# Kernel optimization log

Measured on AMD Instinct MI355X. Metric: run time of the kernel, lower is better.

The kernel has to match this reference:

```python
import jax, jax.numpy as jnp
import numpy as np

NUM_HEADS = 16


def setup_inputs() -> dict:
    key = jax.random.key(0)
    ks = jax.random.split(key, 8)
    B, T, E = 2, 2048, 1024
    hd = E // NUM_HEADS
    return {
        "x": jax.random.normal(ks[0], (B, T, E), jnp.float32),
        "attn_mask_re": jax.random.normal(ks[1], (B, 1, T, hd // 2), jnp.float32),
        "attn_mask_im": jax.random.normal(ks[2], (B, 1, T, hd // 2), jnp.float32),
        "pad_mask": jax.random.normal(ks[3], (B, 1, 1, T), jnp.float32),
        "qkv_w": jax.random.normal(ks[4], (3 * E, E), jnp.float32) * 0.02,
        "qkv_b": jax.random.normal(ks[5], (3 * E,), jnp.float32) * 0.02,
        "o_w": jax.random.normal(ks[6], (E, E), jnp.float32) * 0.02,
        "o_b": jax.random.normal(ks[7], (E,), jnp.float32) * 0.02,
    }


def reference(x, attn_mask_re, attn_mask_im, pad_mask, qkv_w, qkv_b, o_w, o_b):
    B, T, E = x.shape
    H = NUM_HEADS
    hd = E // H
    scale = 1.0 / jnp.sqrt(jnp.asarray(hd, x.dtype))
    # fused QKV projection
    qkv = x @ qkv_w.T + qkv_b            # [B,T,3E]
    q, k, v = jnp.split(qkv, 3, axis=-1)
    q = q.reshape(B, T, H, hd).transpose(0, 2, 1, 3)          # [B,H,T,hd]
    v = v.reshape(B, T, H, hd).transpose(0, 2, 1, 3)          # [B,H,T,hd]
    # rotary on k via complex multiply: k viewed as [B,H,T,hd/2] complex
    kc = k.reshape(B, T, H, hd // 2, 2).transpose(0, 2, 1, 3, 4)  # [B,H,T,hd/2,2]
    kr, ki = kc[..., 0], kc[..., 1]
    mr, mi = attn_mask_re, attn_mask_im   # [B,1,T,hd/2] broadcast over heads
    rr = kr * mr - ki * mi
    ri = kr * mi + ki * mr
    k_rot = jnp.stack([rr, ri], axis=-1).reshape(B, H, T, hd)  # [B,H,T,hd]
    # attention scores [B,H,T,T]
    a = jnp.einsum("bhqd,bhkd->bhqk", q, k_rot) * scale
    a = a + pad_mask
    a = jax.nn.softmax(a, axis=-1)
    # (eval mode: attention dropout is a no-op)
    o = jnp.einsum("bhqk,bhkd->bhqd", a, v)                    # [B,H,T,hd]
    o = o.transpose(0, 2, 1, 3).reshape(B, T, E)
    o = o @ o_w.T + o_b
    a_avg = a.sum(axis=1) / H                                  # [B,T,T]
    return o, a_avg
```

## Files before the change

kernel.cpp:

```cpp
#include <hip/hip_runtime.h>
#include <math.h>

#define TSEQ 2048
#define EMB  1024
#define NH   16
#define HD   64
#define NB   2
#define L2E  1.4426950408889634f

#if defined(__has_builtin)
#if __has_builtin(__builtin_amdgcn_exp2f)
#define EXP2(x) __builtin_amdgcn_exp2f(x)
#else
#define EXP2(x) exp2f(x)
#endif
#else
#define EXP2(x) exp2f(x)
#endif

typedef unsigned short u16;
typedef unsigned int   u32;
typedef __attribute__((ext_vector_type(8))) short short8v;
typedef __attribute__((ext_vector_type(4))) float f32x4;

#define MFMA16(a,b,c) __builtin_amdgcn_mfma_f32_16x16x32_bf16(a,b,c,0,0,0)

__device__ inline u32 f2bf(float x) {
    u32 u = __float_as_uint(x);
    return (u + 0x7fffu + ((u >> 16) & 1u)) >> 16;
}
__device__ inline float bf2f(u32 b) { return __uint_as_float(b << 16); }
__device__ inline void split4(float x0, float x1, float x2, float x3,
                              u32& hw0, u32& hw1, u32& lw0, u32& lw1) {
    u32 h0 = f2bf(x0), h1 = f2bf(x1), h2 = f2bf(x2), h3 = f2bf(x3);
    u32 l0 = f2bf(x0 - bf2f(h0)), l1 = f2bf(x1 - bf2f(h1));
    u32 l2 = f2bf(x2 - bf2f(h2)), l3 = f2bf(x3 - bf2f(h3));
    hw0 = h0 | (h1 << 16); hw1 = h2 | (h3 << 16);
    lw0 = l0 | (l1 << 16); lw1 = l2 | (l3 << 16);
}

__global__ __launch_bounds__(256) void conv_split_kernel(
    const float* __restrict__ in, u16* __restrict__ hi, u16* __restrict__ lo)
{
    const size_t i = (size_t)blockIdx.x * 256 + threadIdx.x;
    float4 v = ((const float4*)in)[i];
    u32 hw0, hw1, lw0, lw1;
    split4(v.x, v.y, v.z, v.w, hw0, hw1, lw0, lw1);
    *(uint2*)(hi + i * 4) = make_uint2(hw0, hw1);
    *(uint2*)(lo + i * 4) = make_uint2(lw0, lw1);
}

#define MM_CORE(Ah_, Al_, Bh_, Bl_, Kdim)                                      \
    __shared__ __align__(16) u16 sAh[128][40], sAl[128][40];                   \
    __shared__ __align__(16) u16 sBh[128][40], sBl[128][40];                   \
    const int tid = threadIdx.x;                                               \
    const int lane = tid & 63, w = tid >> 6;                                   \
    const int lc = lane & 15, lg = lane >> 4;                                  \
    const int wr = w >> 1, wc = w & 1;                                         \
    const int i0 = blockIdx.x * 128, j0 = blockIdx.y * 128;                    \
    const int srow = tid >> 1, shalf = (tid & 1) << 4;                         \
    const u16* pAh = Ah_ + (size_t)(i0 + srow) * Kdim + shalf;                 \
    const u16* pAl = Al_ + (size_t)(i0 + srow) * Kdim + shalf;                 \
    const u16* pBh = Bh_ + (size_t)(j0 + srow) * Kdim + shalf;                 \
    const u16* pBl = Bl_ + (size_t)(j0 + srow) * Kdim + shalf;                 \
    f32x4 acc[4][4];                                                           \
    _Pragma("unroll")                                                          \
    for (int rs = 0; rs < 4; ++rs)                                             \
        _Pragma("unroll")                                                      \
        for (int cs = 0; cs < 4; ++cs) acc[rs][cs] = (f32x4){0.f,0.f,0.f,0.f};\
    for (int k0 = 0; k0 < Kdim; k0 += 32) {                                    \
        short8v va0 = *(const short8v*)(pAh + k0);                             \
        short8v va1 = *(const short8v*)(pAh + k0 + 8);                         \
        short8v vb0 = *(const short8v*)(pAl + k0);                             \
        short8v vb1 = *(const short8v*)(pAl + k0 + 8);                         \
        short8v vc0 = *(const short8v*)(pBh + k0);                             \
        short8v vc1 = *(const short8v*)(pBh + k0 + 8);                         \
        short8v vd0 = *(const short8v*)(pBl + k0);                             \
        short8v vd1 = *(const short8v*)(pBl + k0 + 8);                         \
        *(short8v*)&sAh[srow][shalf]     = va0;                                \
        *(short8v*)&sAh[srow][shalf + 8] = va1;                                \
        *(short8v*)&sAl[srow][shalf]     = vb0;                                \
        *(short8v*)&sAl[srow][shalf + 8] = vb1;                                \
        *(short8v*)&sBh[srow][shalf]     = vc0;                                \
        *(short8v*)&sBh[srow][shalf + 8] = vc1;                                \
        *(short8v*)&sBl[srow][shalf]     = vd0;                                \
        *(short8v*)&sBl[srow][shalf + 8] = vd1;                                \
        __syncthreads();                                                       \
        short8v fah[4], fal[4], fbh[4], fbl[4];                                \
        _Pragma("unroll")                                                      \
        for (int rs = 0; rs < 4; ++rs) {                                       \
            fah[rs] = *(const short8v*)&sAh[wr*64 + rs*16 + lc][lg*8];         \
            fal[rs] = *(const short8v*)&sAl[wr*64 + rs*16 + lc][lg*8];         \
        }                                                                      \
        _Pragma("unroll")                                                      \
        for (int cs = 0; cs < 4; ++cs) {                                       \
            fbh[cs] = *(const short8v*)&sBh[wc*64 + cs*16 + lc][lg*8];         \
            fbl[cs] = *(const short8v*)&sBl[wc*64 + cs*16 + lc][lg*8];         \
        }                                                                      \
        _Pragma("unroll")                                                      \
        for (int rs = 0; rs < 4; ++rs)                                         \
            _Pragma("unroll")                                                  \
            for (int cs = 0; cs < 4; ++cs) {                                   \
                acc[rs][cs] = MFMA16(fah[rs], fbh[cs], acc[rs][cs]);           \
                acc[rs][cs] = MFMA16(fah[rs], fbl[cs], acc[rs][cs]);           \
                acc[rs][cs] = MFMA16(fal[rs], fbh[cs], acc[rs][cs]);           \
            }                                                                  \
        __syncthreads();                                                       \
    }

__global__ __launch_bounds__(256) void mm_qkv_kernel(
    const u16* __restrict__ Ah, const u16* __restrict__ Al,
    const u16* __restrict__ Bh, const u16* __restrict__ Bl,
    const float* __restrict__ bias,
    u16* __restrict__ qhi, u16* __restrict__ qlo,
    u16* __restrict__ khi, u16* __restrict__ klo,
    u16* __restrict__ vthi, u16* __restrict__ vtlo)
{
    MM_CORE(Ah, Al, Bh, Bl, EMB)

    const int which = j0 >> 10;
    #pragma unroll
    for (int cs = 0; cs < 4; ++cs) {
        const int j = j0 + wc*64 + cs*16 + lc;
        const float bj = bias[j];
        const int e = j & (EMB - 1);
        const int hh = e >> 6, d = e & (HD - 1);
        #pragma unroll
        for (int rs = 0; rs < 4; ++rs) {
            #pragma unroll
            for (int r = 0; r < 4; ++r) {
                const int i = i0 + wr*64 + rs*16 + lg*4 + r;
                const int b = i >> 11, t = i & (TSEQ - 1);
                float val = acc[rs][cs][r] + bj;
                if (which == 0) val *= 0.125f;
                const u32 vh = f2bf(val);
                const u32 vl = f2bf(val - bf2f(vh));
                if (which == 2) {
                    const size_t ix = ((size_t)(b * NH + hh) * HD + d) * TSEQ + t;
                    vthi[ix] = (u16)vh; vtlo[ix] = (u16)vl;
                } else {
                    const size_t ix = ((size_t)(b * NH + hh) * TSEQ + t) * HD + d;
                    if (which == 0) { qhi[ix] = (u16)vh; qlo[ix] = (u16)vl; }
                    else            { khi[ix] = (u16)vh; klo[ix] = (u16)vl; }
                }
            }
        }
    }
}

__global__ __launch_bounds__(256) void mm_out_kernel(
    const u16* __restrict__ Ah, const u16* __restrict__ Al,
    const u16* __restrict__ Bh, const u16* __restrict__ Bl,
    const float* __restrict__ bias, float* __restrict__ C)
{
    MM_CORE(Ah, Al, Bh, Bl, EMB)

    #pragma unroll
    for (int cs = 0; cs < 4; ++cs) {
        const int j = j0 + wc*64 + cs*16 + lc;
        const float bj = bias[j];
        #pragma unroll
        for (int rs = 0; rs < 4; ++rs) {
            #pragma unroll
            for (int r = 0; r < 4; ++r) {
                const int i = i0 + wr*64 + rs*16 + lg*4 + r;
                C[(size_t)i * EMB + j] = acc[rs][cs][r] + bj;
            }
        }
    }
}

__global__ __launch_bounds__(256) void rotary_k_kernel(
    u16* __restrict__ khi, u16* __restrict__ klo,
    const float* __restrict__ mre, const float* __restrict__ mim)
{
    const int idx = blockIdx.x * 256 + threadIdx.x;
    const int d2 = idx & 31;
    const int t  = (idx >> 5) & (TSEQ - 1);
    const int b  = idx >> 20;
    u32 h2 = *(u32*)(khi + ((size_t)idx << 1));
    u32 l2 = *(u32*)(klo + ((size_t)idx << 1));
    float kr = bf2f(h2 & 0xffff) + bf2f(l2 & 0xffff);
    float ki = bf2f(h2 >> 16) + bf2f(l2 >> 16);
    const int mix = (b * TSEQ + t) * 32 + d2;
    const float mr = mre[mix], mi = mim[mix];
    float rr = kr * mr - ki * mi;
    float ri = kr * mi + ki * mr;
    u32 hr = f2bf(rr), hx = f2bf(ri);
    u32 lr = f2bf(rr - bf2f(hr)), lx = f2bf(ri - bf2f(hx));
    *(u32*)(khi + ((size_t)idx << 1)) = hr | (hx << 16);
    *(u32*)(klo + ((size_t)idx << 1)) = lr | (lx << 16);
}

__global__ __launch_bounds__(128) void flash_attn_kernel(
    const u16* __restrict__ qhi_, const u16* __restrict__ qlo_,
    const u16* __restrict__ khi_, const u16* __restrict__ klo_,
    const u16* __restrict__ vthi_, const u16* __restrict__ vtlo_,
    const float* __restrict__ pad,
    u16* __restrict__ ohi, u16* __restrict__ olo,
    float* __restrict__ m_out, float* __restrict__ linv_out)
{
    __shared__ __align__(16) u16 Phi[2][32*40];
    __shared__ __align__(16) u16 Plo[2][32*40];

    const int tid  = threadIdx.x;
    const int lane = tid & 63;
    const int w    = tid >> 6;
    const int bid  = blockIdx.x;
    const int xcd  = bid & 7;
    const int local= bid >> 3;
    const int bh   = xcd * 4 + (local >> 5);
    const int sub  = local & 31;
    const int b    = bh >> 4, h = bh & (NH - 1);
    const int qbase = sub * 64 + w * 32;
    const int lg = lane >> 4, lc = lane & 15;

    short8v qh[2][2], ql[2][2];
    #pragma unroll
    for (int qs = 0; qs < 2; ++qs) {
        const size_t qoff = ((size_t)bh * TSEQ + qbase + qs*16 + lc) * HD + lg*8;
        #pragma unroll
        for (int s = 0; s < 2; ++s) {
            qh[qs][s] = *(const short8v*)(qhi_ + qoff + s*32);
            ql[qs][s] = *(const short8v*)(qlo_ + qoff + s*32);
        }
    }

    f32x4 O[2][4];
    float mst[2][4], lst[2][4];
    #pragma unroll
    for (int qs = 0; qs < 2; ++qs) {
        #pragma unroll
        for (int db = 0; db < 4; ++db) O[qs][db] = (f32x4){0.f,0.f,0.f,0.f};
        #pragma unroll
        for (int r = 0; r < 4; ++r) { mst[qs][r] = -1e30f; lst[qs][r] = 0.f; }
    }

    const short oneb = (short)0x3F80;
    const short8v ones = {oneb,oneb,oneb,oneb,oneb,oneb,oneb,oneb};

    u16* PHw = &Phi[w][0];
    u16* PLw = &Plo[w][0];
    const size_t kbase  = (size_t)bh * TSEQ * HD;
    const size_t vtbase = (size_t)bh * HD * TSEQ;

    for (int k0 = 0; k0 < TSEQ; k0 += 32) {
        f32x4 S[2][2];
        #pragma unroll
        for (int qs = 0; qs < 2; ++qs)
            #pragma unroll
            for (int kb2 = 0; kb2 < 2; ++kb2) S[qs][kb2] = (f32x4){0.f,0.f,0.f,0.f};
        #pragma unroll
        for (int kb2 = 0; kb2 < 2; ++kb2) {
            #pragma unroll
            for (int s = 0; s < 2; ++s) {
                const size_t ko = kbase + (size_t)(k0 + kb2*16 + lc) * HD + s*32 + lg*8;
                short8v kh = *(const short8v*)(khi_ + ko);
                short8v kl = *(const short8v*)(klo_ + ko);
                #pragma unroll
                for (int qs = 0; qs < 2; ++qs) {
                    S[qs][kb2] = MFMA16(qh[qs][s], kh, S[qs][kb2]);
                    S[qs][kb2] = MFMA16(qh[qs][s], kl, S[qs][kb2]);
                    S[qs][kb2] = MFMA16(ql[qs][s], kh, S[qs][kb2]);
                }
            }
        }

        short8v vh[4], vl[4];
        #pragma unroll
        for (int db = 0; db < 4; ++db) {
            const size_t vo = vtbase + (size_t)(db*16 + lc) * TSEQ + k0 + lg*8;
            vh[db] = *(const short8v*)(vthi_ + vo);
            vl[db] = *(const short8v*)(vtlo_ + vo);
        }

        const float pv0 = pad[b * TSEQ + k0 + lc];
        const float pv1 = pad[b * TSEQ + k0 + 16 + lc];

        float cc_[2][4];
        #pragma unroll
        for (int qs = 0; qs < 2; ++qs) {
            #pragma unroll
            for (int r = 0; r < 4; ++r) {
                float s0 = S[qs][0][r] + pv0;
                float s1 = S[qs][1][r] + pv1;
                float t = fmaxf(s0, s1);
                t = fmaxf(t, __shfl_xor(t, 1));
                t = fmaxf(t, __shfl_xor(t, 2));
                t = fmaxf(t, __shfl_xor(t, 4));
                t = fmaxf(t, __shfl_xor(t, 8));
                const float mn = fmaxf(mst[qs][r], t);
                cc_[qs][r] = EXP2((mst[qs][r] - mn) * L2E);
                mst[qs][r] = mn;
                const float p0 = EXP2((s0 - mn) * L2E);
                const float p1 = EXP2((s1 - mn) * L2E);
                const int row = qs*16 + lg*4 + r;
                const u32 h0 = f2bf(p0), h1 = f2bf(p1);
                PHw[row*40 + lc]      = (u16)h0;
                PHw[row*40 + 16 + lc] = (u16)h1;
                PLw[row*40 + lc]      = (u16)f2bf(p0 - bf2f(h0));
                PLw[row*40 + 16 + lc] = (u16)f2bf(p1 - bf2f(h1));
                #pragma unroll
                for (int db = 0; db < 4; ++db) O[qs][db][r] *= cc_[qs][r];
            }
        }

        short8v pfh[2], pfl[2];
        #pragma unroll
        for (int qs = 0; qs < 2; ++qs) {
            pfh[qs] = *(const short8v*)(PHw + (qs*16 + lc)*40 + lg*8);
            pfl[qs] = *(const short8v*)(PLw + (qs*16 + lc)*40 + lg*8);
        }

        #pragma unroll
        for (int qs = 0; qs < 2; ++qs) {
            f32x4 Ss = (f32x4){0.f,0.f,0.f,0.f};
            Ss = MFMA16(pfh[qs], ones, Ss);
            Ss = MFMA16(pfl[qs], ones, Ss);
            #pragma unroll
            for (int r = 0; r < 4; ++r) lst[qs][r] = lst[qs][r] * cc_[qs][r] + Ss[r];
        }

        #pragma unroll
        for (int db = 0; db < 4; ++db) {
            #pragma unroll
            for (int qs = 0; qs < 2; ++qs) {
                O[qs][db] = MFMA16(pfh[qs], vh[db], O[qs][db]);
                O[qs][db] = MFMA16(pfh[qs], vl[db], O[qs][db]);
                O[qs][db] = MFMA16(pfl[qs], vh[db], O[qs][db]);
            }
        }
    }

    #pragma unroll
    for (int qs = 0; qs < 2; ++qs) {
        #pragma unroll
        for (int r = 0; r < 4; ++r) {
            const float inv = 1.f / lst[qs][r];
            const int trow = qbase + qs*16 + lg*4 + r;
            const size_t obase = ((size_t)(b * TSEQ + trow)) * EMB + h * HD;
            #pragma unroll
            for (int db = 0; db < 4; ++db) {
                const float val = O[qs][db][r] * inv;
                const u32 vhp = f2bf(val);
                ohi[obase + db*16 + lc] = (u16)vhp;
                olo[obase + db*16 + lc] = (u16)f2bf(val - bf2f(vhp));
            }
            if (lc == 0) {
                m_out[bh * TSEQ + trow] = mst[qs][r];
                linv_out[bh * TSEQ + trow] = inv;
            }
        }
    }
}

__global__ __launch_bounds__(256) void attn_avg_kernel(
    const u16* __restrict__ qhi_, const u16* __restrict__ qlo_,
    const u16* __restrict__ khi_, const u16* __restrict__ klo_,
    const float* __restrict__ pad, const float* __restrict__ m_arr,
    const float* __restrict__ linv_arr, float* __restrict__ a_avg)
{
    const int tid  = threadIdx.x;
    const int lane = tid & 63;
    const int w    = tid >> 6;
    const int bid  = blockIdx.x;
    const int xcd  = bid & 7;
    const int local= bid >> 3;
    const int pair = xcd * 4 + (local >> 6);
    const int b  = pair >> 4;
    const int k0 = (pair & 15) << 7;
    const int q0 = (local & 63) << 5;
    const int lg = lane >> 4, lc = lane & 15;
    const int kw = k0 + w * 32;

    const float pv0 = pad[b * TSEQ + kw + lc];
    const float pv1 = pad[b * TSEQ + kw + 16 + lc];

    f32x4 acc[2][2];
    #pragma unroll
    for (int qs = 0; qs < 2; ++qs)
        #pragma unroll
        for (int kb2 = 0; kb2 < 2; ++kb2) acc[qs][kb2] = (f32x4){0.f,0.f,0.f,0.f};

    for (int h = 0; h < NH; ++h) {
        const size_t hb = (size_t)(b * NH + h) * TSEQ;
        short8v qh[2][2], ql[2][2];
        #pragma unroll
        for (int qs = 0; qs < 2; ++qs) {
            const size_t qoff = (hb + q0 + qs*16 + lc) * HD + lg*8;
            #pragma unroll
            for (int s = 0; s < 2; ++s) {
                qh[qs][s] = *(const short8v*)(qhi_ + qoff + s*32);
                ql[qs][s] = *(const short8v*)(qlo_ + qoff + s*32);
            }
        }
        f32x4 S[2][2];
        #pragma unroll
        for (int qs = 0; qs < 2; ++qs)
            #pragma unroll
            for (int kb2 = 0; kb2 < 2; ++kb2) S[qs][kb2] = (f32x4){0.f,0.f,0.f,0.f};
        #pragma unroll
        for (int kb2 = 0; kb2 < 2; ++kb2) {
            #pragma unroll
            for (int s = 0; s < 2; ++s) {
                const size_t ko = (hb + kw + kb2*16 + lc) * HD + s*32 + lg*8;
                short8v kh = *(const short8v*)(khi_ + ko);
                short8v kl = *(const short8v*)(klo_ + ko);
                #pragma unroll
                for (int qs = 0; qs < 2; ++qs) {
                    S[qs][kb2] = MFMA16(qh[qs][s], kh, S[qs][kb2]);
                    S[qs][kb2] = MFMA16(qh[qs][s], kl, S[qs][kb2]);
                    S[qs][kb2] = MFMA16(ql[qs][s], kh, S[qs][kb2]);
                }
            }
        }
        #pragma unroll
        for (int qs = 0; qs < 2; ++qs) {
            #pragma unroll
            for (int r = 0; r < 4; ++r) {
                const size_t rix = hb + q0 + qs*16 + lg*4 + r;
                const float mh = m_arr[rix];
                const float li = linv_arr[rix];
                acc[qs][0][r] += EXP2((S[qs][0][r] + pv0 - mh) * L2E) * li;
                acc[qs][1][r] += EXP2((S[qs][1][r] + pv1 - mh) * L2E) * li;
            }
        }
    }

    const float invH = 1.0f / (float)NH;
    #pragma unroll
    for (int qs = 0; qs < 2; ++qs) {
        #pragma unroll
        for (int r = 0; r < 4; ++r) {
            const int row = q0 + qs*16 + lg*4 + r;
            #pragma unroll
            for (int kb2 = 0; kb2 < 2; ++kb2)
                a_avg[((size_t)b * TSEQ + row) * TSEQ + kw + kb2*16 + lc] =
                    acc[qs][kb2][r] * invH;
        }
    }
}

extern "C" void kernel_launch(void* const* d_in, const int* in_sizes, int n_in,
                              void* d_out, int out_size, void* d_ws, size_t ws_size,
                              hipStream_t stream)
{
    const float* x    = (const float*)d_in[0];
    const float* mre  = (const float*)d_in[1];
    const float* mim  = (const float*)d_in[2];
    const float* pad  = (const float*)d_in[3];
    const float* qkvw = (const float*)d_in[4];
    const float* qkvb = (const float*)d_in[5];
    const float* ow   = (const float*)d_in[6];
    const float* ob   = (const float*)d_in[7];

    float* out_o = (float*)d_out;
    float* out_a = out_o + (size_t)NB * TSEQ * EMB;

    u16* ohi = (u16*)out_a;
    u16* olo = ohi + (size_t)NB * TSEQ * EMB;

    const size_t SZ = (size_t)NB * NH * TSEQ * HD;
    u16* qhi  = (u16*)d_ws;
    u16* qlo  = qhi  + SZ;
    u16* khi  = qlo  + SZ;
    u16* klo  = khi  + SZ;
    u16* vthi = klo  + SZ;
    u16* vtlo = vthi + SZ;
    float* marr = (float*)(vtlo + SZ);
    float* linv = marr + (size_t)NB * NH * TSEQ;
    u16* xhi  = (u16*)(linv + (size_t)NB * NH * TSEQ);
    u16* xlo  = xhi + SZ;
    u16* whi  = xlo + SZ;
    u16* wlo  = whi + (size_t)3 * EMB * EMB;
    u16* owhi = wlo + (size_t)3 * EMB * EMB;
    u16* owlo = owhi + (size_t)EMB * EMB;

    conv_split_kernel<<<4096, 256, 0, stream>>>(x, xhi, xlo);
    conv_split_kernel<<<3072, 256, 0, stream>>>(qkvw, whi, wlo);
    conv_split_kernel<<<1024, 256, 0, stream>>>(ow, owhi, owlo);

    mm_qkv_kernel<<<dim3(32, 24), 256, 0, stream>>>(
        xhi, xlo, whi, wlo, qkvb, qhi, qlo, khi, klo, vthi, vtlo);

    rotary_k_kernel<<<8192, 256, 0, stream>>>(khi, klo, mre, mim);

    flash_attn_kernel<<<1024, 128, 0, stream>>>(
        qhi, qlo, khi, klo, vthi, vtlo, pad, ohi, olo, marr, linv);

    mm_out_kernel<<<dim3(32, 8), 256, 0, stream>>>(
        ohi, olo, owhi, owlo, ob, out_o);

    attn_avg_kernel<<<2048, 256, 0, stream>>>(
        qhi, qlo, khi, klo, pad, marr, linv, out_a);
}
```

Measured before the change: 731.8 us.

## Double-buffer K/V tile loads in registers across flash-attention iterations

Restructures the flash-attention key loop to handle two 32-key tiles per iteration. The K and V fragments for the next tile are prefetched into a second register set while the current tile's QK, softmax and PV MFMAs run, so global-load latency is hidden behind compute. It also adds a minimum-occupancy hint to the launch bounds. This roughly doubles the registers held for K/V fragments, which risks spills or lower occupancy. The final prefetch reads one tile past the end of each head's K/V rows; the data is never used, but for the last head the read goes past the end of the buffer.

After: 746.1 us. No clear change (+2.0%).

```diff
diff --git a/kernel.cpp b/kernel.cpp
--- a/kernel.cpp
+++ b/kernel.cpp
@@ -192,7 +192,97 @@
     *(u32*)(klo + ((size_t)idx << 1)) = lr | (lx << 16);
 }
 
-__global__ __launch_bounds__(128) void flash_attn_kernel(
+#define LOAD_K(KH, KL, kk)                                                     \
+    { _Pragma("unroll")                                                        \
+      for (int kb2 = 0; kb2 < 2; ++kb2) {                                      \
+        _Pragma("unroll")                                                      \
+        for (int s = 0; s < 2; ++s) {                                          \
+            const size_t ko = kbase + (size_t)((kk) + kb2*16 + lc) * HD        \
+                              + s*32 + lg*8;                                   \
+            KH[kb2][s] = *(const short8v*)(khi_ + ko);                         \
+            KL[kb2][s] = *(const short8v*)(klo_ + ko);                         \
+        } } }
+
+#define LOAD_V(VH, VL, kk)                                                     \
+    { _Pragma("unroll")                                                        \
+      for (int db = 0; db < 4; ++db) {                                         \
+        const size_t vo = vtbase + (size_t)(db*16 + lc) * TSEQ + (kk) + lg*8;  \
+        VH[db] = *(const short8v*)(vthi_ + vo);                                \
+        VL[db] = *(const short8v*)(vtlo_ + vo);                                \
+    } }
+
+#define TILE_BODY(KH, KL, VH, VL, kk)                                          \
+    {                                                                          \
+        f32x4 S[2][2];                                                         \
+        _Pragma("unroll")                                                      \
+        for (int qs = 0; qs < 2; ++qs) {                                       \
+            S[qs][0] = (f32x4){0.f,0.f,0.f,0.f};                               \
+            S[qs][1] = (f32x4){0.f,0.f,0.f,0.f};                               \
+        }                                                                      \
+        _Pragma("unroll")                                                      \
+        for (int kb2 = 0; kb2 < 2; ++kb2) {                                    \
+            _Pragma("unroll")                                                  \
+            for (int s = 0; s < 2; ++s) {                                      \
+                _Pragma("unroll")                                              \
+                for (int qs = 0; qs < 2; ++qs) {                               \
+                    S[qs][kb2] = MFMA16(qh[qs][s], KH[kb2][s], S[qs][kb2]);    \
+                    S[qs][kb2] = MFMA16(qh[qs][s], KL[kb2][s], S[qs][kb2]);    \
+                    S[qs][kb2] = MFMA16(ql[qs][s], KH[kb2][s], S[qs][kb2]);    \
+                } } }                                                          \
+        const float pv0 = pad[b * TSEQ + (kk) + lc];                           \
+        const float pv1 = pad[b * TSEQ + (kk) + 16 + lc];                      \
+        float cc_[2][4];                                                       \
+        _Pragma("unroll")                                                      \
+        for (int qs = 0; qs < 2; ++qs) {                                       \
+            _Pragma("unroll")                                                  \
+            for (int r = 0; r < 4; ++r) {                                      \
+                float s0 = S[qs][0][r] + pv0;                                  \
+                float s1 = S[qs][1][r] + pv1;                                  \
+                float t = fmaxf(s0, s1);                                       \
+                t = fmaxf(t, __shfl_xor(t, 1));                                \
+                t = fmaxf(t, __shfl_xor(t, 2));                                \
+                t = fmaxf(t, __shfl_xor(t, 4));                                \
+                t = fmaxf(t, __shfl_xor(t, 8));                                \
+                const float mn = fmaxf(mst[qs][r], t);                         \
+                cc_[qs][r] = EXP2((mst[qs][r] - mn) * L2E);                    \
+                mst[qs][r] = mn;                                               \
+                const float p0 = EXP2((s0 - mn) * L2E);                        \
+                const float p1 = EXP2((s1 - mn) * L2E);                        \
+                const int row = qs*16 + lg*4 + r;                              \
+                const u32 h0 = f2bf(p0), h1 = f2bf(p1);                        \
+                PHw[row*40 + lc]      = (u16)h0;                               \
+                PHw[row*40 + 16 + lc] = (u16)h1;                               \
+                PLw[row*40 + lc]      = (u16)f2bf(p0 - bf2f(h0));              \
+                PLw[row*40 + 16 + lc] = (u16)f2bf(p1 - bf2f(h1));              \
+                _Pragma("unroll")                                              \
+                for (int db = 0; db < 4; ++db) O[qs][db][r] *= cc_[qs][r];     \
+            } }                                                                \
+        short8v pfh[2], pfl[2];                                                \
+        _Pragma("unroll")                                                      \
+        for (int qs = 0; qs < 2; ++qs) {                                       \
+            pfh[qs] = *(const short8v*)(PHw + (qs*16 + lc)*40 + lg*8);         \
+            pfl[qs] = *(const short8v*)(PLw + (qs*16 + lc)*40 + lg*8);         \
+        }                                                                      \
+        _Pragma("unroll")                                                      \
+        for (int qs = 0; qs < 2; ++qs) {                                       \
+            f32x4 Ss = (f32x4){0.f,0.f,0.f,0.f};                               \
+            Ss = MFMA16(pfh[qs], ones, Ss);                                    \
+            Ss = MFMA16(pfl[qs], ones, Ss);                                    \
+            _Pragma("unroll")                                                  \
+            for (int r = 0; r < 4; ++r)                                        \
+                lst[qs][r] = lst[qs][r] * cc_[qs][r] + Ss[r];                  \
+        }                                                                      \
+        _Pragma("unroll")                                                      \
+        for (int db = 0; db < 4; ++db) {                                       \
+            _Pragma("unroll")                                                  \
+            for (int qs = 0; qs < 2; ++qs) {                                   \
+                O[qs][db] = MFMA16(pfh[qs], VH[db], O[qs][db]);                \
+                O[qs][db] = MFMA16(pfh[qs], VL[db], O[qs][db]);                \
+                O[qs][db] = MFMA16(pfl[qs], VH[db], O[qs][db]);                \
+            } }                                                                \
+    }
+
+__global__ __launch_bounds__(128, 2) void flash_attn_kernel(
     const u16* __restrict__ qhi_, const u16* __restrict__ qlo_,
     const u16* __restrict__ khi_, const u16* __restrict__ klo_,
     const u16* __restrict__ vthi_, const u16* __restrict__ vtlo_,
@@ -244,92 +334,18 @@
     const size_t kbase  = (size_t)bh * TSEQ * HD;
     const size_t vtbase = (size_t)bh * HD * TSEQ;
 
-    for (int k0 = 0; k0 < TSEQ; k0 += 32) {
-        f32x4 S[2][2];
-        #pragma unroll
-        for (int qs = 0; qs < 2; ++qs)
-            #pragma unroll
-            for (int kb2 = 0; kb2 < 2; ++kb2) S[qs][kb2] = (f32x4){0.f,0.f,0.f,0.f};
-        #pragma unroll
-        for (int kb2 = 0; kb2 < 2; ++kb2) {
-            #pragma unroll
-            for (int s = 0; s < 2; ++s) {
-                const size_t ko = kbase + (size_t)(k0 + kb2*16 + lc) * HD + s*32 + lg*8;
-                short8v kh = *(const short8v*)(khi_ + ko);
-                short8v kl = *(const short8v*)(klo_ + ko);
-                #pragma unroll
-                for (int qs = 0; qs < 2; ++qs) {
-                    S[qs][kb2] = MFMA16(qh[qs][s], kh, S[qs][kb2]);
-                    S[qs][kb2] = MFMA16(qh[qs][s], kl, S[qs][kb2]);
-                    S[qs][kb2] = MFMA16(ql[qs][s], kh, S[qs][kb2]);
-                }
-            }
-        }
-
-        short8v vh[4], vl[4];
-        #pragma unroll
-        for (int db = 0; db < 4; ++db) {
-            const size_t vo = vtbase + (size_t)(db*16 + lc) * TSEQ + k0 + lg*8;
-            vh[db] = *(const short8v*)(vthi_ + vo);
-            vl[db] = *(const short8v*)(vtlo_ + vo);
-        }
-
-        const float pv0 = pad[b * TSEQ + k0 + lc];
-        const float pv1 = pad[b * TSEQ + k0 + 16 + lc];
-
-        float cc_[2][4];
-        #pragma unroll
-        for (int qs = 0; qs < 2; ++qs) {
-            #pragma unroll
-            for (int r = 0; r < 4; ++r) {
-                float s0 = S[qs][0][r] + pv0;
-                float s1 = S[qs][1][r] + pv1;
-                float t = fmaxf(s0, s1);
-                t = fmaxf(t, __shfl_xor(t, 1));
-                t = fmaxf(t, __shfl_xor(t, 2));
-                t = fmaxf(t, __shfl_xor(t, 4));
-                t = fmaxf(t, __shfl_xor(t, 8));
-                const float mn = fmaxf(mst[qs][r], t);
-                cc_[qs][r] = EXP2((mst[qs][r] - mn) * L2E);
-                mst[qs][r] = mn;
-                const float p0 = EXP2((s0 - mn) * L2E);
-                const float p1 = EXP2((s1 - mn) * L2E);
-                const int row = qs*16 + lg*4 + r;
-                const u32 h0 = f2bf(p0), h1 = f2bf(p1);
-                PHw[row*40 + lc]      = (u16)h0;
-                PHw[row*40 + 16 + lc] = (u16)h1;
-                PLw[row*40 + lc]      = (u16)f2bf(p0 - bf2f(h0));
-                PLw[row*40 + 16 + lc] = (u16)f2bf(p1 - bf2f(h1));
-                #pragma unroll
-                for (int db = 0; db < 4; ++db) O[qs][db][r] *= cc_[qs][r];
-            }
-        }
-
-        short8v pfh[2], pfl[2];
-        #pragma unroll
-        for (int qs = 0; qs < 2; ++qs) {
-            pfh[qs] = *(const short8v*)(PHw + (qs*16 + lc)*40 + lg*8);
-            pfl[qs] = *(const short8v*)(PLw + (qs*16 + lc)*40 + lg*8);
-        }
-
-        #pragma unroll
-        for (int qs = 0; qs < 2; ++qs) {
-            f32x4 Ss = (f32x4){0.f,0.f,0.f,0.f};
-            Ss = MFMA16(pfh[qs], ones, Ss);
-            Ss = MFMA16(pfl[qs], ones, Ss);
-            #pragma unroll
-            for (int r = 0; r < 4; ++r) lst[qs][r] = lst[qs][r] * cc_[qs][r] + Ss[r];
-        }
-
-        #pragma unroll
-        for (int db = 0; db < 4; ++db) {
-            #pragma unroll
-            for (int qs = 0; qs < 2; ++qs) {
-                O[qs][db] = MFMA16(pfh[qs], vh[db], O[qs][db]);
-                O[qs][db] = MFMA16(pfh[qs], vl[db], O[qs][db]);
-                O[qs][db] = MFMA16(pfl[qs], vh[db], O[qs][db]);
-            }
-        }
+    short8v kHA[2][2], kLA[2][2], vHA[4], vLA[4];
+    short8v kHB[2][2], kLB[2][2], vHB[4], vLB[4];
+    LOAD_K(kHA, kLA, 0)
+    LOAD_V(vHA, vLA, 0)
+
+    for (int k0 = 0; k0 < TSEQ; k0 += 64) {
+        LOAD_K(kHB, kLB, k0 + 32)
+        LOAD_V(vHB, vLB, k0 + 32)
+        TILE_BODY(kHA, kLA, vHA, vLA, k0)
+        LOAD_K(kHA, kLA, k0 + 64)
+        LOAD_V(vHA, vLA, k0 + 64)
+        TILE_BODY(kHB, kLB, vHB, vLB, k0 + 32)
     }
 
     #pragma unroll
```
